# Performance work log

Measured on AMD Instinct MI355X. Metric: run time of the kernel, lower is better.

The kernel has to match this reference:

```python
import jax, jax.numpy as jnp
import numpy as np

D_MODEL = 256
D_ENC_M = 256  # mel encoder dim (keys/values), sets temperature = sqrt(D_ENC_M)
D_ENC_T = 256  # text encoder dim (queries)
LN_EPS = 1e-5


def setup_inputs() -> dict:
    key = jax.random.key(0)
    ks = jax.random.split(key, 9)
    B, MEL_LEN, SRC_LEN = 16, 2048, 512
    mel_encoding = jax.random.normal(ks[0], (B, MEL_LEN, D_ENC_M), dtype=jnp.float32)
    text_encoding = jax.random.normal(ks[1], (B, SRC_LEN, D_ENC_T), dtype=jnp.float32)
    mel_mask = jax.random.randint(ks[2], (B, MEL_LEN), 0, 2).astype(bool)
    src_mask = jax.random.randint(ks[3], (B, SRC_LEN), 0, 2).astype(bool)
    # Linear weights (no bias), xavier-uniform style scale
    def xavier(k, shape):
        fan_in, fan_out = shape[1], shape[0]
        lim = jnp.sqrt(6.0 / (fan_in + fan_out))
        return jax.random.uniform(k, shape, jnp.float32, -lim, lim)
    Wq = xavier(ks[4], (D_MODEL, D_ENC_T))
    Wk = xavier(ks[5], (D_MODEL, D_ENC_M))
    Wv = xavier(ks[6], (D_MODEL, D_ENC_M))
    gamma = jnp.ones((D_MODEL,), jnp.float32)
    beta = jnp.zeros((D_MODEL,), jnp.float32)
    return {"mel_encoding": mel_encoding, "text_encoding": text_encoding,
            "mel_mask": mel_mask, "src_mask": src_mask,
            "Wq": Wq, "Wk": Wk, "Wv": Wv, "gamma": gamma, "beta": beta}


def reference(mel_encoding, text_encoding, mel_mask, src_mask, Wq, Wk, Wv, gamma, beta):
    # QKV projections (nn.Linear, bias=False): y = x @ W^T
    q = jnp.einsum('btd,md->btm', text_encoding, Wq)   # [B, src_len, d_model]
    k = jnp.einsum('bsd,md->bsm', mel_encoding, Wk)    # [B, mel_len, d_model]
    v = jnp.einsum('bsd,md->bsm', mel_encoding, Wv)    # [B, mel_len, d_model]
    temperature = jnp.asarray(D_ENC_M, jnp.float32) ** 0.5
    attn = jnp.einsum('btm,bsm->bts', q, k) / temperature  # [B, src_len, mel_len]
    # pre-softmax fill over mel (key) padding
    attn = jnp.where(mel_mask[:, None, :], -jnp.inf, attn)
    attn = jax.nn.softmax(attn, axis=2)
    # post-softmax zeroing over src (query) padding
    attn = jnp.where(src_mask[:, :, None], 0.0, attn)
    output = jnp.einsum('bts,bsm->btm', attn, v)  # [B, src_len, d_model]
    # dropout is identity in eval mode; LayerNorm over last dim
    mu = jnp.mean(output, axis=-1, keepdims=True)
    var = jnp.mean(jnp.square(output - mu), axis=-1, keepdims=True)
    output = (output - mu) * jax.lax.rsqrt(var + LN_EPS) * gamma + beta
    return (output, attn)
```

## Files before the change

kernel.cpp:

```cpp
#include <hip/hip_runtime.h>
#include <hip/hip_bf16.h>
#include <stdint.h>

#define DMODEL 256
#define BATCH  16
#define MEL    2048
#define SRC    512

typedef __attribute__((ext_vector_type(8))) short bf16x8;
typedef __attribute__((ext_vector_type(4))) short short4v;
typedef __attribute__((ext_vector_type(4))) float f32x4;
typedef __attribute__((ext_vector_type(4))) int   i32x4;

__device__ inline short f2bf(float f) {
    union { float f; uint32_t u; } c{f};
    uint32_t u = c.u;
    u += 0x7FFFu + ((u >> 16) & 1u);
    return (short)(u >> 16);
}

__device__ inline bf16x8 cvt8(const float* p) {
    const f32x4* q = reinterpret_cast<const f32x4*>(p);
    f32x4 a = q[0], b = q[1];
    bf16x8 r;
    r[0] = f2bf(a[0]); r[1] = f2bf(a[1]); r[2] = f2bf(a[2]); r[3] = f2bf(a[3]);
    r[4] = f2bf(b[0]); r[5] = f2bf(b[1]); r[6] = f2bf(b[2]); r[7] = f2bf(b[7-4]);
    r[7] = f2bf(b[3]);
    r[6] = f2bf(b[2]);
    return r;
}

__global__ __launch_bounds__(256)
void proj_all_kernel(const float* __restrict__ mel, const float* __restrict__ text,
                     const float* __restrict__ Wq, const float* __restrict__ Wk,
                     const float* __restrict__ Wv,
                     short* __restrict__ qbf, short* __restrict__ kbf,
                     short* __restrict__ vt) {
    __shared__ char SMEM[36864];
    short* As = (short*)SMEM;
    short* Bs = (short*)SMEM + 128 * 72;

    const int tid = threadIdx.x;
    const int lane = tid & 63, w = tid >> 6;
    const int lr = lane & 15, lk = lane >> 4;
    const int wr = w >> 1, wc = w & 1;

    const int u = blockIdx.x;
    const float *Af, *Bf; short* C; int ldc; size_t arow0, brow0;
    if (u < 128) {
        arow0 = (size_t)(u >> 1) * 128; brow0 = (size_t)(u & 1) * 128;
        Af = text; Bf = Wq; C = qbf; ldc = DMODEL;
    } else if (u < 640) {
        int v = u - 128;
        arow0 = (size_t)(v >> 1) * 128; brow0 = (size_t)(v & 1) * 128;
        Af = mel; Bf = Wk; C = kbf; ldc = DMODEL;
    } else {
        int v = u - 640;
        int xcd = v & 7, j = v >> 3;
        int b = 2 * xcd + (j >> 5), t = j & 31;
        arow0 = (size_t)(t & 1) * 128; brow0 = (size_t)(t >> 1) * 128;
        Af = Wv; Bf = mel + (size_t)b * MEL * DMODEL;
        C = vt + (size_t)b * DMODEL * MEL; ldc = MEL;
    }
    C += arow0 * ldc + brow0;

    bf16x8 sA[4], sB[4];
    auto STAGE = [&](int kt) {
#pragma unroll
        for (int i = 0; i < 4; ++i) {
            int idx = i * 256 + tid;
            int row = idx >> 3, c8 = (idx & 7) * 8;
            sA[i] = cvt8(Af + (arow0 + row) * 256 + kt * 64 + c8);
            sB[i] = cvt8(Bf + (brow0 + row) * 256 + kt * 64 + c8);
        }
    };

    STAGE(0);
    f32x4 acc[4][4];
#pragma unroll
    for (int m = 0; m < 4; ++m)
#pragma unroll
        for (int n = 0; n < 4; ++n) acc[m][n] = (f32x4){0.f, 0.f, 0.f, 0.f};

    for (int kt = 0; kt < 4; ++kt) {
        __syncthreads();
#pragma unroll
        for (int i = 0; i < 4; ++i) {
            int idx = i * 256 + tid;
            int row = idx >> 3, c8 = (idx & 7) * 8;
            *(bf16x8*)&As[row * 72 + c8] = sA[i];
            *(bf16x8*)&Bs[row * 72 + c8] = sB[i];
        }
        __syncthreads();
        if (kt < 3) STAGE(kt + 1);
#pragma unroll
        for (int kt2 = 0; kt2 < 2; ++kt2) {
            bf16x8 af[4], bfr[4];
#pragma unroll
            for (int m = 0; m < 4; ++m)
                af[m] = *(const bf16x8*)&As[(64 * wr + 16 * m + lr) * 72 + kt2 * 32 + 8 * lk];
#pragma unroll
            for (int n = 0; n < 4; ++n)
                bfr[n] = *(const bf16x8*)&Bs[(64 * wc + 16 * n + lr) * 72 + kt2 * 32 + 8 * lk];
#pragma unroll
            for (int m = 0; m < 4; ++m)
#pragma unroll
                for (int n = 0; n < 4; ++n)
                    acc[m][n] = __builtin_amdgcn_mfma_f32_16x16x32_bf16(af[m], bfr[n], acc[m][n], 0, 0, 0);
        }
    }

    __syncthreads();
    short* Cs = (short*)SMEM;
#pragma unroll
    for (int m = 0; m < 4; ++m)
#pragma unroll
        for (int n = 0; n < 4; ++n)
#pragma unroll
            for (int r = 0; r < 4; ++r)
                Cs[(64 * wr + 16 * m + 4 * lk + r) * 136 + 64 * wc + 16 * n + lr] =
                    f2bf(acc[m][n][r]);
    __syncthreads();
#pragma unroll
    for (int i = 0; i < 8; ++i) {
        int idx = i * 256 + tid;
        int row = idx >> 4, c8 = (idx & 15) * 8;
        *(bf16x8*)&C[(size_t)row * ldc + c8] = *(const bf16x8*)&Cs[row * 136 + c8];
    }
}

__global__ __launch_bounds__(256)
void sgemm_kernel(const short* __restrict__ qbf, const short* __restrict__ kbf,
                  float* __restrict__ attn) {
    __shared__ char SMEM[36864];
    short* As = (short*)SMEM;
    short* Bs = (short*)SMEM + 128 * 72;

    const int tid = threadIdx.x;
    const int lane = tid & 63, w = tid >> 6;
    const int lr = lane & 15, lk = lane >> 4;
    const int wr = w >> 1, wc = w & 1;

    const int bid = blockIdx.x;
    const int xcd = bid & 7, j = bid >> 3;
    const int z = 2 * xcd + (j >> 6);
    const int t = j & 63;
    const int x = t & 3, y = t >> 2;

    const short* A = qbf + (size_t)z * SRC * DMODEL + (size_t)x * 128 * DMODEL;
    const short* B = kbf + (size_t)z * MEL * DMODEL + (size_t)y * 128 * DMODEL;
    float* Cw = attn + (size_t)z * SRC * MEL + (size_t)x * 128 * MEL + (size_t)y * 128;

    bf16x8 sA[4], sB[4];
    auto STAGE = [&](int kt) {
#pragma unroll
        for (int i = 0; i < 4; ++i) {
            int idx = i * 256 + tid;
            int row = idx >> 3, c8 = (idx & 7) * 8;
            sA[i] = *(const bf16x8*)(A + (size_t)row * DMODEL + kt * 64 + c8);
            sB[i] = *(const bf16x8*)(B + (size_t)row * DMODEL + kt * 64 + c8);
        }
    };

    STAGE(0);
    f32x4 acc[4][4];
#pragma unroll
    for (int m = 0; m < 4; ++m)
#pragma unroll
        for (int n = 0; n < 4; ++n) acc[m][n] = (f32x4){0.f, 0.f, 0.f, 0.f};

    for (int kt = 0; kt < 4; ++kt) {
        __syncthreads();
#pragma unroll
        for (int i = 0; i < 4; ++i) {
            int idx = i * 256 + tid;
            int row = idx >> 3, c8 = (idx & 7) * 8;
            *(bf16x8*)&As[row * 72 + c8] = sA[i];
            *(bf16x8*)&Bs[row * 72 + c8] = sB[i];
        }
        __syncthreads();
        if (kt < 3) STAGE(kt + 1);
#pragma unroll
        for (int kt2 = 0; kt2 < 2; ++kt2) {
            bf16x8 af[4], bfr[4];
#pragma unroll
            for (int m = 0; m < 4; ++m)
                af[m] = *(const bf16x8*)&As[(64 * wr + 16 * m + lr) * 72 + kt2 * 32 + 8 * lk];
#pragma unroll
            for (int n = 0; n < 4; ++n)
                bfr[n] = *(const bf16x8*)&Bs[(64 * wc + 16 * n + lr) * 72 + kt2 * 32 + 8 * lk];
#pragma unroll
            for (int m = 0; m < 4; ++m)
#pragma unroll
                for (int n = 0; n < 4; ++n)
                    acc[m][n] = __builtin_amdgcn_mfma_f32_16x16x32_bf16(af[m], bfr[n], acc[m][n], 0, 0, 0);
        }
    }

    __syncthreads();
    float* Cs = (float*)SMEM;
#pragma unroll
    for (int half = 0; half < 2; ++half) {
        if (wr == half) {
#pragma unroll
            for (int m = 0; m < 4; ++m)
#pragma unroll
                for (int n = 0; n < 4; ++n)
#pragma unroll
                    for (int r = 0; r < 4; ++r)
                        Cs[(16 * m + 4 * lk + r) * 132 + 64 * wc + 16 * n + lr] =
                            acc[m][n][r] * 0.0625f;
        }
        __syncthreads();
#pragma unroll
        for (int i = 0; i < 8; ++i) {
            int idx = i * 256 + tid;
            int row = idx >> 5, c4 = (idx & 31) * 4;
            *(f32x4*)&Cw[(size_t)(half * 64 + row) * MEL + c4] = *(const f32x4*)&Cs[row * 132 + c4];
        }
        __syncthreads();
    }
}

__global__ __launch_bounds__(512)
void softmax_kernel(float* __restrict__ attn, const int* __restrict__ mel_mask,
                    const int* __restrict__ src_mask) {
    const int w = threadIdx.x >> 6, lane = threadIdx.x & 63;
    const int row = blockIdx.x * 8 + w;
    const int b = row >> 9, t = row & 511;
    float* p = attn + (size_t)row * MEL + lane * 32;
    const i32x4* mm = (const i32x4*)(mel_mask + b * MEL + lane * 32);

    f32x4 v[8]; i32x4 m[8];
#pragma unroll
    for (int j = 0; j < 8; ++j) { v[j] = ((const f32x4*)p)[j]; m[j] = mm[j]; }

    float mx = -3.0e38f;
#pragma unroll
    for (int j = 0; j < 8; ++j)
#pragma unroll
        for (int e = 0; e < 4; ++e) if (!m[j][e]) mx = fmaxf(mx, v[j][e]);
#pragma unroll
    for (int off = 32; off; off >>= 1) mx = fmaxf(mx, __shfl_xor(mx, off));

    float sum = 0.f;
#pragma unroll
    for (int j = 0; j < 8; ++j)
#pragma unroll
        for (int e = 0; e < 4; ++e) {
            float ev = m[j][e] ? 0.f : __expf(v[j][e] - mx);
            v[j][e] = ev; sum += ev;
        }
#pragma unroll
    for (int off = 32; off; off >>= 1) sum += __shfl_xor(sum, off);

    const float inv = src_mask[b * SRC + t] ? 0.f : 1.f / sum;
#pragma unroll
    for (int j = 0; j < 8; ++j) {
        f32x4 o = { v[j][0] * inv, v[j][1] * inv, v[j][2] * inv, v[j][3] * inv };
        ((f32x4*)p)[j] = o;
    }
}

__global__ __launch_bounds__(512)
void pv_ln_kernel(const float* __restrict__ attn, const short* __restrict__ vt,
                  const float* __restrict__ gamma, const float* __restrict__ beta,
                  float* __restrict__ out) {
    __shared__ char SMEM[42496];
    short* As = (short*)SMEM;
    short* Bs = (short*)(SMEM + 4608);
    float* red = (float*)(SMEM + 41472);
    float* Ost = (float*)(SMEM + 4608);

    const int tid = threadIdx.x;
    const int lane = tid & 63, w = tid >> 6;
    const int lr = lane & 15, lk = lane >> 4;
    const int wr = w >> 2, wc = w & 3;

    const int bid = blockIdx.x;
    const int xcd = bid & 7, j = bid >> 3;
    const int b = 2 * xcd + (j >> 4);
    const int mt = j & 15;
    const size_t row0 = (size_t)mt * 32;

    const float* A = attn + (size_t)b * SRC * MEL + row0 * MEL;
    const short* Bv = vt + (size_t)b * DMODEL * MEL;

    float gm[4], bt[4];
#pragma unroll
    for (int n = 0; n < 4; ++n) {
        gm[n] = gamma[64 * wc + 16 * n + lr];
        bt[n] = beta[64 * wc + 16 * n + lr];
    }

    f32x4 sAv; bf16x8 sB[4];
    const int a_row = tid >> 4, a_c4 = (tid & 15) * 4;
    auto STAGE = [&](int kt) {
        sAv = *(const f32x4*)(A + (size_t)a_row * MEL + kt * 64 + a_c4);
#pragma unroll
        for (int i = 0; i < 4; ++i) {
            int idx = i * 512 + tid;
            int row = idx >> 3, c8 = (idx & 7) * 8;
            sB[i] = *(const bf16x8*)(Bv + (size_t)row * MEL + kt * 64 + c8);
        }
    };

    STAGE(0);
    f32x4 acc[4];
#pragma unroll
    for (int n = 0; n < 4; ++n) acc[n] = (f32x4){0.f, 0.f, 0.f, 0.f};

    for (int kt = 0; kt < MEL / 64; ++kt) {
        __syncthreads();
        {
            short4v a4 = { f2bf(sAv[0]), f2bf(sAv[1]), f2bf(sAv[2]), f2bf(sAv[3]) };
            *(short4v*)&As[a_row * 72 + a_c4] = a4;
#pragma unroll
            for (int i = 0; i < 4; ++i) {
                int idx = i * 512 + tid;
                int row = idx >> 3, c8 = (idx & 7) * 8;
                *(bf16x8*)&Bs[row * 72 + c8] = sB[i];
            }
        }
        __syncthreads();
        if (kt + 1 < MEL / 64) STAGE(kt + 1);
#pragma unroll
        for (int kt2 = 0; kt2 < 2; ++kt2) {
            bf16x8 af = *(const bf16x8*)&As[(16 * wr + lr) * 72 + kt2 * 32 + 8 * lk];
#pragma unroll
            for (int n = 0; n < 4; ++n) {
                bf16x8 bfr = *(const bf16x8*)&Bs[(64 * wc + 16 * n + lr) * 72 + kt2 * 32 + 8 * lk];
                acc[n] = __builtin_amdgcn_mfma_f32_16x16x32_bf16(af, bfr, acc[n], 0, 0, 0);
            }
        }
    }

    float s1[4] = {0.f, 0.f, 0.f, 0.f}, s2[4] = {0.f, 0.f, 0.f, 0.f};
#pragma unroll
    for (int n = 0; n < 4; ++n)
#pragma unroll
        for (int r = 0; r < 4; ++r) {
            s1[r] += acc[n][r];
            s2[r] += acc[n][r] * acc[n][r];
        }
#pragma unroll
    for (int off = 8; off; off >>= 1)
#pragma unroll
        for (int r = 0; r < 4; ++r) {
            s1[r] += __shfl_xor(s1[r], off);
            s2[r] += __shfl_xor(s2[r], off);
        }
    __syncthreads();
    if (lr == 0) {
#pragma unroll
        for (int r = 0; r < 4; ++r) {
            red[(16 * wr + 4 * lk + r) * 4 + wc] = s1[r];
            red[128 + (16 * wr + 4 * lk + r) * 4 + wc] = s2[r];
        }
    }
    __syncthreads();
    float mu[4], rsig[4];
#pragma unroll
    for (int r = 0; r < 4; ++r) {
        int rowi = 16 * wr + 4 * lk + r;
        float S1 = red[rowi * 4 + 0] + red[rowi * 4 + 1] + red[rowi * 4 + 2] + red[rowi * 4 + 3];
        float S2 = red[128 + rowi * 4 + 0] + red[128 + rowi * 4 + 1] +
                   red[128 + rowi * 4 + 2] + red[128 + rowi * 4 + 3];
        mu[r] = S1 * (1.f / DMODEL);
        rsig[r] = rsqrtf(S2 * (1.f / DMODEL) - mu[r] * mu[r] + 1e-5f);
    }
    __syncthreads();
#pragma unroll
    for (int n = 0; n < 4; ++n)
#pragma unroll
        for (int r = 0; r < 4; ++r)
            Ost[(16 * wr + 4 * lk + r) * 260 + 64 * wc + 16 * n + lr] =
                (acc[n][r] - mu[r]) * rsig[r] * gm[n] + bt[n];
    __syncthreads();
#pragma unroll
    for (int i = 0; i < 4; ++i) {
        int idx = i * 512 + tid;
        int row = idx >> 6, c4 = (idx & 63) * 4;
        *(f32x4*)&out[((size_t)b * SRC + row0 + row) * DMODEL + c4] =
            *(const f32x4*)&Ost[row * 260 + c4];
    }
}

extern "C" void kernel_launch(void* const* d_in, const int* in_sizes, int n_in,
                              void* d_out, int out_size, void* d_ws, size_t ws_size,
                              hipStream_t stream) {
    const float* mel      = (const float*)d_in[0];
    const float* text     = (const float*)d_in[1];
    const int*   mel_mask = (const int*)d_in[2];
    const int*   src_mask = (const int*)d_in[3];
    const float* Wq       = (const float*)d_in[4];
    const float* Wk       = (const float*)d_in[5];
    const float* Wv       = (const float*)d_in[6];
    const float* gamma    = (const float*)d_in[7];
    const float* beta     = (const float*)d_in[8];

    float* out  = (float*)d_out;
    float* attn = out + (size_t)BATCH * SRC * DMODEL;

    short* qbf = (short*)d_ws;
    short* kbf = qbf + (size_t)BATCH * SRC * DMODEL;
    short* vt  = kbf + (size_t)BATCH * MEL * DMODEL;

    proj_all_kernel<<<1152, 256, 0, stream>>>(mel, text, Wq, Wk, Wv, qbf, kbf, vt);
    sgemm_kernel<<<1024, 256, 0, stream>>>(qbf, kbf, attn);
    softmax_kernel<<<BATCH * SRC / 8, 512, 0, stream>>>(attn, mel_mask, src_mask);
    pv_ln_kernel<<<256, 512, 0, stream>>>(attn, vt, gamma, beta, out);
}
```

Measured before the change: 225.1 us.

## Fuse softmax statistics into QK GEMM epilogue and normalize inside PV kernel

Result: faster. 202.9 us (-9.9%).

```diff
diff --git a/kernel.cpp b/kernel.cpp
--- a/kernel.cpp
+++ b/kernel.cpp
@@ -10,7 +10,6 @@
 typedef __attribute__((ext_vector_type(8))) short bf16x8;
 typedef __attribute__((ext_vector_type(4))) short short4v;
 typedef __attribute__((ext_vector_type(4))) float f32x4;
-typedef __attribute__((ext_vector_type(4))) int   i32x4;
 
 __device__ inline short f2bf(float f) {
     union { float f; uint32_t u; } c{f};
@@ -24,9 +23,7 @@
     f32x4 a = q[0], b = q[1];
     bf16x8 r;
     r[0] = f2bf(a[0]); r[1] = f2bf(a[1]); r[2] = f2bf(a[2]); r[3] = f2bf(a[3]);
-    r[4] = f2bf(b[0]); r[5] = f2bf(b[1]); r[6] = f2bf(b[2]); r[7] = f2bf(b[7-4]);
-    r[7] = f2bf(b[3]);
-    r[6] = f2bf(b[2]);
+    r[4] = f2bf(b[0]); r[5] = f2bf(b[1]); r[6] = f2bf(b[2]); r[7] = f2bf(b[3]);
     return r;
 }
 
@@ -46,23 +43,34 @@
     const int wr = w >> 1, wc = w & 1;
 
     const int u = blockIdx.x;
-    const float *Af, *Bf; short* C; int ldc; size_t arow0, brow0;
-    if (u < 128) {
-        arow0 = (size_t)(u >> 1) * 128; brow0 = (size_t)(u & 1) * 128;
+    const int xcd = u & 7, slot = u >> 3;
+
+    const float *Af, *Bf; short* C; int ldc;
+    size_t aro, bro, coff;
+    if (slot < 128) {
+        const int g = slot >> 2, m = slot & 3;
+        const int st = 32 * xcd + g;
+        const int b = st >> 4;
+        const size_t mr0 = (size_t)(st & 15) * 128;
+        if (m < 2) {
+            aro = (size_t)b * MEL + mr0;
+            bro = (size_t)m * 128;
+            Af = mel; Bf = Wk; C = kbf; ldc = DMODEL;
+            coff = aro * DMODEL + bro;
+        } else {
+            aro = (size_t)(m - 2) * 128;
+            bro = (size_t)b * MEL + mr0;
+            Af = Wv; Bf = mel; C = vt + (size_t)b * DMODEL * MEL; ldc = MEL;
+            coff = aro * MEL + mr0;
+        }
+    } else {
+        const int qi = 16 * xcd + (slot - 128);
+        aro = (size_t)(qi >> 1) * 128;
+        bro = (size_t)(qi & 1) * 128;
         Af = text; Bf = Wq; C = qbf; ldc = DMODEL;
-    } else if (u < 640) {
-        int v = u - 128;
-        arow0 = (size_t)(v >> 1) * 128; brow0 = (size_t)(v & 1) * 128;
-        Af = mel; Bf = Wk; C = kbf; ldc = DMODEL;
-    } else {
-        int v = u - 640;
-        int xcd = v & 7, j = v >> 3;
-        int b = 2 * xcd + (j >> 5), t = j & 31;
-        arow0 = (size_t)(t & 1) * 128; brow0 = (size_t)(t >> 1) * 128;
-        Af = Wv; Bf = mel + (size_t)b * MEL * DMODEL;
-        C = vt + (size_t)b * DMODEL * MEL; ldc = MEL;
-    }
-    C += arow0 * ldc + brow0;
+        coff = aro * DMODEL + bro;
+    }
+    C += coff;
 
     bf16x8 sA[4], sB[4];
     auto STAGE = [&](int kt) {
@@ -70,8 +78,8 @@
         for (int i = 0; i < 4; ++i) {
             int idx = i * 256 + tid;
             int row = idx >> 3, c8 = (idx & 7) * 8;
-            sA[i] = cvt8(Af + (arow0 + row) * 256 + kt * 64 + c8);
-            sB[i] = cvt8(Bf + (brow0 + row) * 256 + kt * 64 + c8);
+            sA[i] = cvt8(Af + (aro + row) * 256 + kt * 64 + c8);
+            sB[i] = cvt8(Bf + (bro + row) * 256 + kt * 64 + c8);
         }
     };
 
@@ -131,7 +139,9 @@
 
 __global__ __launch_bounds__(256)
 void sgemm_kernel(const short* __restrict__ qbf, const short* __restrict__ kbf,
-                  float* __restrict__ attn) {
+                  const int* __restrict__ mel_mask,
+                  float* __restrict__ attn,
+                  float* __restrict__ pmax, float* __restrict__ psum) {
     __shared__ char SMEM[36864];
     short* As = (short*)SMEM;
     short* Bs = (short*)SMEM + 128 * 72;
@@ -197,6 +207,11 @@
         }
     }
 
+    bool msk[4];
+#pragma unroll
+    for (int n = 0; n < 4; ++n)
+        msk[n] = mel_mask[z * MEL + y * 128 + 64 * wc + 16 * n + lr] != 0;
+
     __syncthreads();
     float* Cs = (float*)SMEM;
 #pragma unroll
@@ -209,7 +224,7 @@
 #pragma unroll
                     for (int r = 0; r < 4; ++r)
                         Cs[(16 * m + 4 * lk + r) * 132 + 64 * wc + 16 * n + lr] =
-                            acc[m][n][r] * 0.0625f;
+                            msk[n] ? -1e30f : acc[m][n][r] * 0.0625f;
         }
         __syncthreads();
 #pragma unroll
@@ -218,53 +233,57 @@
             int row = idx >> 5, c4 = (idx & 31) * 4;
             *(f32x4*)&Cw[(size_t)(half * 64 + row) * MEL + c4] = *(const f32x4*)&Cs[row * 132 + c4];
         }
+        {
+            const int rrow = tid >> 2, seg = tid & 3;
+            const f32x4* crow = (const f32x4*)(Cs + rrow * 132 + seg * 32);
+            float m8 = -3.0e38f;
+#pragma unroll
+            for (int jj = 0; jj < 8; ++jj) {
+                f32x4 v = crow[jj];
+#pragma unroll
+                for (int e = 0; e < 4; ++e) m8 = fmaxf(m8, v[e]);
+            }
+            m8 = fmaxf(m8, __shfl_xor(m8, 1));
+            m8 = fmaxf(m8, __shfl_xor(m8, 2));
+            float s8 = 0.f;
+#pragma unroll
+            for (int jj = 0; jj < 8; ++jj) {
+                f32x4 v = crow[jj];
+#pragma unroll
+                for (int e = 0; e < 4; ++e) s8 += __expf(v[e] - m8);
+            }
+            s8 += __shfl_xor(s8, 1);
+            s8 += __shfl_xor(s8, 2);
+            if (seg == 0) {
+                int grow = z * SRC + x * 128 + half * 64 + rrow;
+                pmax[y * 8192 + grow] = m8;
+                psum[y * 8192 + grow] = s8;
+            }
+        }
         __syncthreads();
     }
 }
 
 __global__ __launch_bounds__(512)
-void softmax_kernel(float* __restrict__ attn, const int* __restrict__ mel_mask,
-                    const int* __restrict__ src_mask) {
-    const int w = threadIdx.x >> 6, lane = threadIdx.x & 63;
-    const int row = blockIdx.x * 8 + w;
-    const int b = row >> 9, t = row & 511;
-    float* p = attn + (size_t)row * MEL + lane * 32;
-    const i32x4* mm = (const i32x4*)(mel_mask + b * MEL + lane * 32);
-
-    f32x4 v[8]; i32x4 m[8];
-#pragma unroll
-    for (int j = 0; j < 8; ++j) { v[j] = ((const f32x4*)p)[j]; m[j] = mm[j]; }
-
-    float mx = -3.0e38f;
-#pragma unroll
-    for (int j = 0; j < 8; ++j)
-#pragma unroll
-        for (int e = 0; e < 4; ++e) if (!m[j][e]) mx = fmaxf(mx, v[j][e]);
-#pragma unroll
-    for (int off = 32; off; off >>= 1) mx = fmaxf(mx, __shfl_xor(mx, off));
-
-    float sum = 0.f;
-#pragma unroll
-    for (int j = 0; j < 8; ++j)
-#pragma unroll
-        for (int e = 0; e < 4; ++e) {
-            float ev = m[j][e] ? 0.f : __expf(v[j][e] - mx);
-            v[j][e] = ev; sum += ev;
-        }
-#pragma unroll
-    for (int off = 32; off; off >>= 1) sum += __shfl_xor(sum, off);
-
-    const float inv = src_mask[b * SRC + t] ? 0.f : 1.f / sum;
-#pragma unroll
-    for (int j = 0; j < 8; ++j) {
-        f32x4 o = { v[j][0] * inv, v[j][1] * inv, v[j][2] * inv, v[j][3] * inv };
-        ((f32x4*)p)[j] = o;
-    }
+void rowred_kernel(const float* __restrict__ pmax, const float* __restrict__ psum,
+                   const int* __restrict__ src_mask,
+                   float* __restrict__ Mrow, float* __restrict__ Minv) {
+    const int row = blockIdx.x * 512 + threadIdx.x;
+    float M = -3.0e38f;
+#pragma unroll
+    for (int i = 0; i < 16; ++i) M = fmaxf(M, pmax[i * 8192 + row]);
+    float Z = 0.f;
+#pragma unroll
+    for (int i = 0; i < 16; ++i)
+        Z += psum[i * 8192 + row] * __expf(pmax[i * 8192 + row] - M);
+    Mrow[row] = M;
+    Minv[row] = (src_mask[row] || !(Z > 0.f)) ? 0.f : 1.f / Z;
 }
 
 __global__ __launch_bounds__(512)
-void pv_ln_kernel(const float* __restrict__ attn, const short* __restrict__ vt,
+void pv_ln_kernel(float* __restrict__ attn, const short* __restrict__ vt,
                   const float* __restrict__ gamma, const float* __restrict__ beta,
+                  const float* __restrict__ Mrow, const float* __restrict__ Minv,
                   float* __restrict__ out) {
     __shared__ char SMEM[42496];
     short* As = (short*)SMEM;
@@ -283,7 +302,7 @@
     const int mt = j & 15;
     const size_t row0 = (size_t)mt * 32;
 
-    const float* A = attn + (size_t)b * SRC * MEL + row0 * MEL;
+    float* A = attn + (size_t)b * SRC * MEL + row0 * MEL;
     const short* Bv = vt + (size_t)b * DMODEL * MEL;
 
     float gm[4], bt[4];
@@ -293,8 +312,11 @@
         bt[n] = beta[64 * wc + 16 * n + lr];
     }
 
+    const int a_row = tid >> 4, a_c4 = (tid & 15) * 4;
+    const float Mr = Mrow[(size_t)b * SRC + row0 + a_row];
+    const float Iv = Minv[(size_t)b * SRC + row0 + a_row];
+
     f32x4 sAv; bf16x8 sB[4];
-    const int a_row = tid >> 4, a_c4 = (tid & 15) * 4;
     auto STAGE = [&](int kt) {
         sAv = *(const f32x4*)(A + (size_t)a_row * MEL + kt * 64 + a_c4);
 #pragma unroll
@@ -313,7 +335,11 @@
     for (int kt = 0; kt < MEL / 64; ++kt) {
         __syncthreads();
         {
-            short4v a4 = { f2bf(sAv[0]), f2bf(sAv[1]), f2bf(sAv[2]), f2bf(sAv[3]) };
+            f32x4 p;
+#pragma unroll
+            for (int e = 0; e < 4; ++e) p[e] = __expf(sAv[e] - Mr) * Iv;
+            *(f32x4*)(A + (size_t)a_row * MEL + kt * 64 + a_c4) = p;
+            short4v a4 = { f2bf(p[0]), f2bf(p[1]), f2bf(p[2]), f2bf(p[3]) };
             *(short4v*)&As[a_row * 72 + a_c4] = a4;
 #pragma unroll
             for (int i = 0; i < 4; ++i) {
@@ -405,9 +431,13 @@
     short* qbf = (short*)d_ws;
     short* kbf = qbf + (size_t)BATCH * SRC * DMODEL;
     short* vt  = kbf + (size_t)BATCH * MEL * DMODEL;
+    float* pmax = (float*)(vt + (size_t)BATCH * DMODEL * MEL);
+    float* psum = pmax + 16 * 8192;
+    float* Mrow = psum + 16 * 8192;
+    float* Minv = Mrow + 8192;
 
     proj_all_kernel<<<1152, 256, 0, stream>>>(mel, text, Wq, Wk, Wv, qbf, kbf, vt);
-    sgemm_kernel<<<1024, 256, 0, stream>>>(qbf, kbf, attn);
-    softmax_kernel<<<BATCH * SRC / 8, 512, 0, stream>>>(attn, mel_mask, src_mask);
-    pv_ln_kernel<<<256, 512, 0, stream>>>(attn, vt, gamma, beta, out);
-}
+    sgemm_kernel<<<1024, 256, 0, stream>>>(qbf, kbf, mel_mask, attn, pmax, psum);
+    rowred_kernel<<<16, 512, 0, stream>>>(pmax, psum, src_mask, Mrow, Minv);
+    pv_ln_kernel<<<256, 512, 0, stream>>>(attn, vt, gamma, beta, Mrow, Minv, out);
+}
```
